# Optimization experiments

Hardware: AMD Instinct MI355X
Metric: run time of the kernel (lower is better)

Reference implementation:

```python
import jax, jax.numpy as jnp
import numpy as np

E = 5        # num_experts
K = 2        # top-k routing
DIM = 768    # token dim
HID = 3072   # dim * mlp_ratio
T = 16384    # num tokens (batch*seq collapsed, per SparseDispatcher contract)
EPS = float(np.finfo(np.float64).eps)  # np.finfo(float).eps used in combine


def setup_inputs() -> dict:
    key = jax.random.key(0)
    ks = jax.random.split(key, 5)
    x = jax.random.normal(ks[0], (T, DIM), jnp.float32)
    # w_gate is nn.Parameter(zeros) in the source; randomize so routing is non-trivial
    w_gate = jax.random.normal(ks[1], (DIM, E), jnp.float32) * 0.02
    # stacked ExpertMLP params (fc1: dim->hid, fc2: hid->dim), small init per init_weights
    W1 = jax.random.normal(ks[2], (E, DIM, HID), jnp.float32) * 0.02
    b1 = jnp.zeros((E, HID), jnp.float32)
    W2 = jax.random.normal(ks[3], (E, HID, DIM), jnp.float32) * 0.02
    b2 = jnp.zeros((E, DIM), jnp.float32)
    return {"x": x, "w_gate": w_gate, "W1": W1, "b1": b1, "W2": W2, "b2": b2}


def reference(x, w_gate, W1, b1, W2, b2):
    # --- noisy top-k gating, eval mode (no noise added at inference) ---
    logits = x @ w_gate                              # [T, E]
    top_vals, top_idx = jax.lax.top_k(logits, K)     # [T, K]
    top_gates = jax.nn.softmax(top_vals, axis=-1)    # softmax over selected logits
    tok = jnp.arange(x.shape[0])[:, None]
    gates = jnp.zeros_like(logits).at[tok, top_idx].set(top_gates)  # sparse [T, E]

    # --- dispatch / expert MLP / combine ---
    # SparseDispatcher.combine: combined[b] = log(sum_e gate[b,e] * exp(expert_e(x[b])))
    # (zeros where no expert contributes are replaced by eps before log)
    acc = jnp.zeros((x.shape[0], DIM), jnp.float32)
    for e in range(E):  # small fixed expert count; dense-equivalent of sparse dispatch
        h = jax.nn.gelu(x @ W1[e] + b1[e], approximate=False)  # torch nn.GELU (erf)
        y = h @ W2[e] + b2[e]                                   # [T, DIM]
        acc = acc + gates[:, e:e + 1] * jnp.exp(y)
    return jnp.log(jnp.where(acc == 0.0, EPS, acc))
```

## Files before the change

### kernel.cpp

```cpp
#include <hip/hip_runtime.h>
#include <math.h>

#define T_TOK 16384
#define DIM   768
#define HID   3072
#define NE    5
#define MT    65
#define HCAP  (MT * 128)
#define CSTR  32
#define EPSF  2.2204460492503131e-16f

typedef short bf16x8  __attribute__((ext_vector_type(8)));
typedef float f32x4   __attribute__((ext_vector_type(4)));
typedef float f32x16  __attribute__((ext_vector_type(16)));

#define MFMA16(A, B, C) __builtin_amdgcn_mfma_f32_16x16x32_bf16((A), (B), (C), 0, 0, 0)
#define MFMA32(A, B, C) __builtin_amdgcn_mfma_f32_32x32x16_bf16((A), (B), (C), 0, 0, 0)

__device__ __forceinline__ unsigned short f2bf(float f) {
    unsigned int u = __float_as_uint(f);
    unsigned int r = (u + 0x7fffu + ((u >> 16) & 1u)) >> 16;
    return (unsigned short)r;
}

__device__ __forceinline__ void gld16(const void* g, void* l) {
    __builtin_amdgcn_global_load_lds(
        (const __attribute__((address_space(1))) void*)g,
        (__attribute__((address_space(3))) void*)l, 16, 0, 0);
}

__global__ void prep_w1p(const float* __restrict__ W1, unsigned short* __restrict__ W1p) {
    int idx = blockIdx.x * 256 + threadIdx.x;
    if (idx >= NE * 24 * 12 * 128 * 8) return;
    int p = idx & 7;
    int n = (idx >> 3) & 127;
    int t = idx >> 10;
    int kb = t % 12; t /= 12;
    int nb = t % 24; int e = t / 24;
    int klog = kb * 64 + (p ^ (n & 7)) * 8;
    const float* src = W1 + ((size_t)e * DIM + klog) * HID + nb * 128 + n;
    bf16x8 v;
    #pragma unroll
    for (int j = 0; j < 8; ++j) v[j] = (short)f2bf(src[(size_t)j * HID]);
    *reinterpret_cast<bf16x8*>(W1p + (size_t)idx * 8) = v;
}

__global__ void prep_w2p(const float* __restrict__ W2, unsigned short* __restrict__ W2p) {
    int idx = blockIdx.x * 256 + threadIdx.x;
    if (idx >= NE * 6 * 48 * 128 * 8) return;
    int p = idx & 7;
    int n = (idx >> 3) & 127;
    int t = idx >> 10;
    int kb = t % 48; t /= 48;
    int nb = t % 6; int e = t / 6;
    int klog = kb * 64 + (p ^ (n & 7)) * 8;
    const float* src = W2 + ((size_t)e * HID + klog) * DIM + nb * 128 + n;
    bf16x8 v;
    #pragma unroll
    for (int j = 0; j < 8; ++j) v[j] = (short)f2bf(src[(size_t)j * DIM]);
    *reinterpret_cast<bf16x8*>(W2p + (size_t)idx * 8) = v;
}

__global__ __launch_bounds__(256) void gate_kernel(
    const float* __restrict__ x, const float* __restrict__ wg,
    unsigned short* __restrict__ xb, int* __restrict__ counts,
    int* __restrict__ btok, float* __restrict__ bgate) {
    __shared__ int   s_e[2][64];
    __shared__ float s_g[2][64];
    __shared__ int   lcnt[NE];
    __shared__ int   gbase[NE];

    const int tid = threadIdx.x;
    if (tid < NE) lcnt[tid] = 0;
    const int grp = tid >> 4, l16 = tid & 15;
    const int t0 = blockIdx.x * 64 + grp * 4;

    double acc[4][NE];
    #pragma unroll
    for (int tt = 0; tt < 4; ++tt)
        #pragma unroll
        for (int e = 0; e < NE; ++e) acc[tt][e] = 0.0;

    for (int i = 0; i < 12; ++i) {
        const int dbase = i * 64 + l16 * 4;
        float4 xv[4];
        #pragma unroll
        for (int tt = 0; tt < 4; ++tt) {
            xv[tt] = *reinterpret_cast<const float4*>(x + (size_t)(t0 + tt) * DIM + dbase);
            ushort4 o;
            o.x = f2bf(xv[tt].x); o.y = f2bf(xv[tt].y);
            o.z = f2bf(xv[tt].z); o.w = f2bf(xv[tt].w);
            *reinterpret_cast<ushort4*>(xb + (size_t)(t0 + tt) * DIM + dbase) = o;
        }
        #pragma unroll
        for (int j = 0; j < 4; ++j) {
            const int d = dbase + j;
            float w0 = wg[d * NE + 0], w1 = wg[d * NE + 1], w2 = wg[d * NE + 2];
            float w3 = wg[d * NE + 3], w4 = wg[d * NE + 4];
            #pragma unroll
            for (int tt = 0; tt < 4; ++tt) {
                double xd = (double)((&xv[tt].x)[j]);
                acc[tt][0] += xd * (double)w0;
                acc[tt][1] += xd * (double)w1;
                acc[tt][2] += xd * (double)w2;
                acc[tt][3] += xd * (double)w3;
                acc[tt][4] += xd * (double)w4;
            }
        }
    }
    #pragma unroll
    for (int off = 8; off; off >>= 1)
        #pragma unroll
        for (int tt = 0; tt < 4; ++tt)
            #pragma unroll
            for (int e = 0; e < NE; ++e)
                acc[tt][e] += __shfl_down(acc[tt][e], off, 16);

    if (l16 == 0) {
        #pragma unroll
        for (int tt = 0; tt < 4; ++tt) {
            double v[NE] = {acc[tt][0], acc[tt][1], acc[tt][2], acc[tt][3], acc[tt][4]};
            int i0 = 0;
            for (int e = 1; e < NE; ++e) if (v[e] > v[i0]) i0 = e;
            int i1 = -1;
            for (int e = 0; e < NE; ++e) {
                if (e == i0) continue;
                if (i1 < 0 || v[e] > v[i1]) i1 = e;
            }
            float e1 = expf((float)(v[i1] - v[i0]));
            float g0 = 1.0f / (1.0f + e1);
            int li = grp * 4 + tt;
            s_e[0][li] = i0;  s_g[0][li] = g0;
            s_e[1][li] = i1;  s_g[1][li] = e1 * g0;
        }
    }
    __syncthreads();

    int mye = 0, myoff = 0, mytok = 0;
    float myg = 0.0f;
    if (tid < 128) {
        int li = tid >> 1, which = tid & 1;
        mye = s_e[which][li];
        myg = s_g[which][li];
        mytok = blockIdx.x * 64 + li;
        myoff = atomicAdd(&lcnt[mye], 1);
    }
    __syncthreads();
    if (tid < NE) gbase[tid] = atomicAdd(&counts[tid * CSTR], lcnt[tid]);
    __syncthreads();
    if (tid < 128) {
        int p = gbase[mye] + myoff;
        btok[mye * T_TOK + p] = mytok;
        bgate[mye * T_TOK + p] = myg;
    }
}

__global__ __launch_bounds__(256, 3) void combo_kernel(
    const unsigned short* __restrict__ xb,
    const unsigned short* __restrict__ W1p,
    const unsigned short* __restrict__ W2p,
    const float* __restrict__ b1, const float* __restrict__ b2,
    const int* __restrict__ counts, const int* __restrict__ btok,
    const float* __restrict__ bgate,
    unsigned short* __restrict__ h0, unsigned short* __restrict__ h1,
    float* __restrict__ out, int g1e, int g2e) {
    __shared__ __align__(16) unsigned short As[128 * 64];
    __shared__ __align__(16) unsigned short Bs[128 * 64];
    __shared__ int   sst[128];
    __shared__ float ssg[128];

    const int g2n = (g2e >= 0) ? MT * 6 : 0;
    int bx = blockIdx.x;
    const bool isG2 = bx < g2n;
    int e, mt, nt;
    if (isG2) { e = g2e; mt = bx / 6;  nt = bx % 6; }
    else      { bx -= g2n; e = g1e; mt = bx / 24; nt = bx % 24; }
    const int cnt = counts[e * CSTR];
    const int m0 = mt * 128;
    if (m0 >= cnt) return;
    unsigned short* hbuf = (e & 1) ? h1 : h0;

    const int tid = threadIdx.x;
    const int wv = tid >> 6, lane = tid & 63;
    const int wm = wv >> 1, wn = wv & 1;
    const int col = lane & 15, quad = lane >> 4;
    const int l8 = lane & 7, r8 = lane >> 3;

    const unsigned short* aptr[4];
    if (isG2) {
        if (tid < 128) {
            int pos = m0 + tid;
            sst[tid] = (pos < cnt) ? btok[e * T_TOK + pos] : 0;
            ssg[tid] = (pos < cnt) ? bgate[e * T_TOK + pos] : 0.0f;
        }
        #pragma unroll
        for (int q = 0; q < 4; ++q) {
            int r = wv * 32 + q * 8 + r8;
            aptr[q] = hbuf + (size_t)(m0 + r) * HID + (l8 ^ r8) * 8;
        }
    } else {
        #pragma unroll
        for (int q = 0; q < 4; ++q) {
            int r = wv * 32 + q * 8 + r8;
            int pos = m0 + r;
            int tok = btok[e * T_TOK + (pos < cnt ? pos : 0)];
            aptr[q] = xb + (size_t)tok * DIM + (l8 ^ r8) * 8;
        }
    }
    const unsigned short* btile = isG2
        ? W2p + ((size_t)(e * 6 + nt)) * 48 * 8192
        : W1p + ((size_t)(e * 24 + nt)) * 12 * 8192;
    const int ksteps = isG2 ? 48 : 12;

    f32x4 acc[4][4];
    #pragma unroll
    for (int i = 0; i < 4; ++i)
        #pragma unroll
        for (int j = 0; j < 4; ++j)
            acc[i][j] = (f32x4){0.f, 0.f, 0.f, 0.f};

    for (int ks = 0; ks < ksteps; ++ks) {
        const unsigned short* bk = btile + (size_t)ks * 8192 + (size_t)wv * 2048 + lane * 8;
        #pragma unroll
        for (int q = 0; q < 4; ++q)
            gld16(aptr[q] + ks * 64, &As[(wv * 4 + q) * 512]);
        #pragma unroll
        for (int q = 0; q < 4; ++q)
            gld16(bk + q * 512, &Bs[(wv * 4 + q) * 512]);
        __syncthreads();
        #pragma unroll
        for (int kf = 0; kf < 2; ++kf) {
            const int p = ((kf * 4 + quad) ^ l8) * 8;
            bf16x8 a[4], b[4];
            #pragma unroll
            for (int i = 0; i < 4; ++i)
                a[i] = *reinterpret_cast<const bf16x8*>(&As[(wm * 64 + i * 16 + col) * 64 + p]);
            #pragma unroll
            for (int i = 0; i < 4; ++i)
                b[i] = *reinterpret_cast<const bf16x8*>(&Bs[(wn * 64 + i * 16 + col) * 64 + p]);
            #pragma unroll
            for (int i = 0; i < 4; ++i)
                #pragma unroll
                for (int j = 0; j < 4; ++j)
                    acc[i][j] = MFMA16(a[i], b[j], acc[i][j]);
        }
        __syncthreads();
    }

    const int nb0 = nt * 128 + wn * 64;
    if (!isG2) {
        #pragma unroll
        for (int j = 0; j < 4; ++j) {
            float bias = b1[e * HID + nb0 + j * 16 + col];
            #pragma unroll
            for (int i = 0; i < 4; ++i) {
                #pragma unroll
                for (int r = 0; r < 4; ++r) {
                    int row = m0 + wm * 64 + i * 16 + quad * 4 + r;
                    float v = acc[i][j][r] + bias;
                    float gl = 0.5f * v * (1.0f + erff(v * 0.70710678118654752f));
                    hbuf[(size_t)row * HID + nb0 + j * 16 + col] = f2bf(gl);
                }
            }
        }
    } else {
        #pragma unroll
        for (int j = 0; j < 4; ++j) {
            float bias = b2[e * DIM + nb0 + j * 16 + col];
            #pragma unroll
            for (int i = 0; i < 4; ++i) {
                #pragma unroll
                for (int r = 0; r < 4; ++r) {
                    int lrow = wm * 64 + i * 16 + quad * 4 + r;
                    float g = ssg[lrow];
                    if (g > 0.0f) {
                        float v = acc[i][j][r] + bias;
                        atomicAdd(out + (size_t)sst[lrow] * DIM + nb0 + j * 16 + col,
                                  g * expf(v));
                    }
                }
            }
        }
    }
}

__global__ void log_kernel(float* __restrict__ out, int n) {
    int i = blockIdx.x * 256 + threadIdx.x;
    if (i < n) {
        float v = out[i];
        out[i] = logf(v == 0.0f ? EPSF : v);
    }
}

__global__ void prep_w1_v2(const float* __restrict__ W1, unsigned short* __restrict__ W1s) {
    int g = blockIdx.x * 4 + (threadIdx.x >> 6);
    int lane = threadIdx.x & 63;
    int kf = g % 48;
    int rest = g / 48;
    int nt2 = rest % 96;
    int e = rest / 96;
    int n = nt2 * 32 + (lane & 31);
    int k0 = kf * 16 + (lane >> 5) * 8;
    const float* src = W1 + ((size_t)e * DIM + k0) * HID + n;
    bf16x8 v;
    #pragma unroll
    for (int j = 0; j < 8; ++j) v[j] = (short)f2bf(src[(size_t)j * HID]);
    *reinterpret_cast<bf16x8*>(W1s + ((size_t)g * 64 + lane) * 8) = v;
}

__global__ void prep_w2_v2(const float* __restrict__ W2, unsigned short* __restrict__ W2s) {
    int g = blockIdx.x * 4 + (threadIdx.x >> 6);
    int lane = threadIdx.x & 63;
    int kf = g % 192;
    int rest = g / 192;
    int nt2 = rest % 24;
    int e = rest / 24;
    int n = nt2 * 32 + (lane & 31);
    int k0 = kf * 16 + (lane >> 5) * 8;
    const float* src = W2 + ((size_t)e * HID + k0) * DIM + n;
    bf16x8 v;
    #pragma unroll
    for (int j = 0; j < 8; ++j) v[j] = (short)f2bf(src[(size_t)j * DIM]);
    *reinterpret_cast<bf16x8*>(W2s + ((size_t)g * 64 + lane) * 8) = v;
}

__global__ __launch_bounds__(512, 2) void expert_v2(
    const unsigned short* __restrict__ xb, const unsigned short* __restrict__ W1s,
    const unsigned short* __restrict__ W2s, const float* __restrict__ b1,
    const float* __restrict__ b2, const int* __restrict__ counts,
    const int* __restrict__ btok, const float* __restrict__ bgate,
    float* __restrict__ out) {
    __shared__ __align__(16) unsigned short xs[64][776];
    __shared__ __align__(16) unsigned short hs[2][64][136];
    __shared__ int   st[64];
    __shared__ float sg[64];

    const int e = blockIdx.y;
    const int cnt = counts[e * CSTR];
    const int m0 = blockIdx.x * 64;
    if (m0 >= cnt) return;

    const int tid = threadIdx.x;
    const int wv = tid >> 6, lane = tid & 63;
    const int l31 = lane & 31, lhi = lane >> 5;

    if (tid < 64) {
        int pos = m0 + tid;
        st[tid] = (pos < cnt) ? btok[e * T_TOK + pos] : 0;
        sg[tid] = (pos < cnt) ? bgate[e * T_TOK + pos] : 0.0f;
    }
    __syncthreads();
    {
        int r = tid >> 3, seg = tid & 7;
        const unsigned short* src = xb + (size_t)st[r] * DIM + seg * 96;
        unsigned short* dst = &xs[r][seg * 96];
        #pragma unroll
        for (int i = 0; i < 12; ++i)
            reinterpret_cast<bf16x8*>(dst)[i] = reinterpret_cast<const bf16x8*>(src)[i];
    }
    __syncthreads();

    const int mt2 = wv & 1, nt2l = wv >> 1;
    f32x16 acc[2][3];
    #pragma unroll
    for (int a_ = 0; a_ < 2; ++a_)
        #pragma unroll
        for (int b_ = 0; b_ < 3; ++b_)
            #pragma unroll
            for (int q = 0; q < 16; ++q) acc[a_][b_][q] = 0.0f;

    const unsigned short* arow = &xs[mt2 * 32 + l31][lhi * 8];
    for (int jc = 0; jc < 24; ++jc) {
        f32x16 c0, c1;
        #pragma unroll
        for (int q = 0; q < 16; ++q) { c0[q] = 0.0f; c1[q] = 0.0f; }
        const unsigned short* bpa =
            W1s + ((size_t)((e * 96 + jc * 4 + nt2l) * 48)) * 512 + lane * 8;
        #pragma unroll
        for (int kf = 0; kf < 48; kf += 2) {
            bf16x8 a0 = *reinterpret_cast<const bf16x8*>(arow + kf * 16);
            bf16x8 b0 = *reinterpret_cast<const bf16x8*>(bpa + (size_t)kf * 512);
            c0 = MFMA32(a0, b0, c0);
            bf16x8 a1 = *reinterpret_cast<const bf16x8*>(arow + kf * 16 + 16);
            bf16x8 b1 = *reinterpret_cast<const bf16x8*>(bpa + (size_t)kf * 512 + 512);
            c1 = MFMA32(a1, b1, c1);
        }
        #pragma unroll
        for (int q = 0; q < 16; ++q) c0[q] += c1[q];
        {
            int colc = nt2l * 32 + l31;
            float bias = b1[e * HID + jc * 128 + colc];
            #pragma unroll
            for (int reg = 0; reg < 16; ++reg) {
                int row = (reg & 3) + 8 * (reg >> 2) + 4 * lhi;
                float v = c0[reg] + bias;
                float gl = 0.5f * v * (1.0f + erff(v * 0.70710678118654752f));
                hs[jc & 1][mt2 * 32 + row][colc] = f2bf(gl);
            }
        }
        __syncthreads();
        const unsigned short* bpb =
            W2s + ((size_t)((e * 24 + wv * 3) * 192 + jc * 8)) * 512 + lane * 8;
        #pragma unroll
        for (int kf = 0; kf < 8; ++kf) {
            bf16x8 af0 = *reinterpret_cast<const bf16x8*>(&hs[jc & 1][l31][kf * 16 + lhi * 8]);
            bf16x8 af1 = *reinterpret_cast<const bf16x8*>(&hs[jc & 1][32 + l31][kf * 16 + lhi * 8]);
            #pragma unroll
            for (int i = 0; i < 3; ++i) {
                bf16x8 bv = *reinterpret_cast<const bf16x8*>(bpb + ((size_t)i * 192 + kf) * 512);
                acc[0][i] = MFMA32(af0, bv, acc[0][i]);
                acc[1][i] = MFMA32(af1, bv, acc[1][i]);
            }
        }
    }
    #pragma unroll
    for (int mt = 0; mt < 2; ++mt) {
        #pragma unroll
        for (int i = 0; i < 3; ++i) {
            int cg = (wv * 3 + i) * 32 + l31;
            float bias2 = b2[e * DIM + cg];
            #pragma unroll
            for (int reg = 0; reg < 16; ++reg) {
                int row = mt * 32 + (reg & 3) + 8 * (reg >> 2) + 4 * lhi;
                float g = sg[row];
                if (g > 0.0f) {
                    float v = acc[mt][i][reg] + bias2;
                    atomicAdd(out + (size_t)st[row] * DIM + cg, g * expf(v));
                }
            }
        }
    }
}


extern "C" void kernel_launch(void* const* d_in, const int* in_sizes, int n_in,
                              void* d_out, int out_size, void* d_ws, size_t ws_size,
                              hipStream_t stream) {
    const float* x  = (const float*)d_in[0];
    const float* wg = (const float*)d_in[1];
    const float* W1 = (const float*)d_in[2];
    const float* b1 = (const float*)d_in[3];
    const float* W2 = (const float*)d_in[4];
    const float* b2 = (const float*)d_in[5];
    float* out = (float*)d_out;

    char* ws = (char*)d_ws;
    int*            counts = (int*)ws;
    int*            btok   = (int*)(ws + 1024);
    float*          bgate  = (float*)(ws + 1024 + 327680);
    unsigned short* xb     = (unsigned short*)(ws + 1024 + 2 * 327680);
    unsigned short* W1b    = xb + (size_t)T_TOK * DIM;
    unsigned short* W2b    = W1b + (size_t)NE * DIM * HID;
    unsigned short* h0     = W2b + (size_t)NE * HID * DIM;
    unsigned short* h1     = h0 + (size_t)HCAP * HID;

    const size_t need_fast = 1024 + 2 * 327680
        + (size_t)T_TOK * DIM * 2 + 2 * (size_t)NE * DIM * HID * 2
        + 2 * (size_t)HCAP * HID * 2;
    const bool fast = ws_size >= need_fast;

    hipMemsetAsync(counts, 0, 1024, stream);
    hipMemsetAsync(out, 0, (size_t)out_size * sizeof(float), stream);

    gate_kernel<<<T_TOK / 64, 256, 0, stream>>>(x, wg, xb, counts, btok, bgate);

    if (fast) {
        prep_w1p<<<(NE * 24 * 12 * 128 * 8 + 255) / 256, 256, 0, stream>>>(W1, W1b);
        prep_w2p<<<(NE * 6 * 48 * 128 * 8 + 255) / 256, 256, 0, stream>>>(W2, W2b);
        for (int s = 0; s < 6; ++s) {
            int g1e = (s <= 4) ? s : -1;
            int g2e = s - 1;
            int nb = (g2e >= 0 ? MT * 6 : 0) + (g1e >= 0 ? MT * 24 : 0);
            combo_kernel<<<nb, 256, 0, stream>>>(xb, W1b, W2b, b1, b2, counts,
                                                 btok, bgate, h0, h1, out, g1e, g2e);
        }
    } else {
        prep_w1_v2<<<NE * 96 * 48 / 4, 256, 0, stream>>>(W1, W1b);
        prep_w2_v2<<<NE * 24 * 192 / 4, 256, 0, stream>>>(W2, W2b);
        expert_v2<<<dim3(T_TOK / 64, NE), 512, 0, stream>>>(
            xb, W1b, W2b, b1, b2, counts, btok, bgate, out);
    }

    log_kernel<<<(out_size + 255) / 256, 256, 0, stream>>>(out, out_size);
}
```

Measured before the change: 716.5 us.

## Triple-buffer LDS pipeline with 256-row tiles and 512-thread blocks in expert GEMM

Raises the expert GEMM tile from 128 to 256 token rows using 8 waves per block. It adds a three-stage LDS ring buffer so global-to-LDS loads for step k+2 overlap the MFMA work on step k, synchronised with explicit vmcnt waits and barriers. It also remaps block indices so that consecutive blocks are spread across tiles, and raises wave priority around the compute phase. The goal is to hide memory latency and improve weight reuse per block. In exchange it uses more LDS per block, allows fewer blocks per CU, and leaves larger tail tiles when experts receive uneven token counts.

New measurement: 885.0 us. 23.5% more time.

```diff
diff --git a/kernel.cpp b/kernel.cpp
--- a/kernel.cpp
+++ b/kernel.cpp
@@ -5,8 +5,10 @@
 #define DIM   768
 #define HID   3072
 #define NE    5
-#define MT    65
-#define HCAP  (MT * 128)
+#define MT2   32
+#define HCAP  (MT2 * 256)
+#define G1NT  24
+#define G2NT  6
 #define CSTR  32
 #define EPSF  2.2204460492503131e-16f
 
@@ -155,7 +157,7 @@
     }
 }
 
-__global__ __launch_bounds__(256, 3) void combo_kernel(
+__global__ __launch_bounds__(512, 2) void combo_kernel(
     const unsigned short* __restrict__ xb,
     const unsigned short* __restrict__ W1p,
     const unsigned short* __restrict__ W2p,
@@ -164,19 +166,27 @@
     const float* __restrict__ bgate,
     unsigned short* __restrict__ h0, unsigned short* __restrict__ h1,
     float* __restrict__ out, int g1e, int g2e) {
-    __shared__ __align__(16) unsigned short As[128 * 64];
-    __shared__ __align__(16) unsigned short Bs[128 * 64];
-    __shared__ int   sst[128];
-    __shared__ float ssg[128];
-
-    const int g2n = (g2e >= 0) ? MT * 6 : 0;
+    __shared__ __align__(16) unsigned short As[3][256 * 64];
+    __shared__ __align__(16) unsigned short Bs[3][128 * 64];
+    __shared__ int   sst[256];
+    __shared__ float ssg[256];
+
+    const int g2n = (g2e >= 0) ? MT2 * G2NT : 0;
     int bx = blockIdx.x;
     const bool isG2 = bx < g2n;
     int e, mt, nt;
-    if (isG2) { e = g2e; mt = bx / 6;  nt = bx % 6; }
-    else      { bx -= g2n; e = g1e; mt = bx / 24; nt = bx % 24; }
+    if (isG2) {
+        e = g2e;
+        int w = (bx & 7) * (g2n >> 3) + (bx >> 3);
+        mt = w / G2NT; nt = w % G2NT;
+    } else {
+        bx -= g2n;
+        e = g1e;
+        int w = (bx & 7) * ((MT2 * G1NT) >> 3) + (bx >> 3);
+        mt = w / G1NT; nt = w % G1NT;
+    }
     const int cnt = counts[e * CSTR];
-    const int m0 = mt * 128;
+    const int m0 = mt * 256;
     if (m0 >= cnt) return;
     unsigned short* hbuf = (e & 1) ? h1 : h0;
 
@@ -188,7 +198,7 @@
 
     const unsigned short* aptr[4];
     if (isG2) {
-        if (tid < 128) {
+        if (tid < 256) {
             int pos = m0 + tid;
             sst[tid] = (pos < cnt) ? btok[e * T_TOK + pos] : 0;
             ssg[tid] = (pos < cnt) ? bgate[e * T_TOK + pos] : 0.0f;
@@ -208,9 +218,19 @@
         }
     }
     const unsigned short* btile = isG2
-        ? W2p + ((size_t)(e * 6 + nt)) * 48 * 8192
-        : W1p + ((size_t)(e * 24 + nt)) * 12 * 8192;
+        ? W2p + ((size_t)(e * G2NT + nt)) * 48 * 8192
+        : W1p + ((size_t)(e * G1NT + nt)) * 12 * 8192;
+    const unsigned short* bsrc = btile + (size_t)wv * 1024 + lane * 8;
     const int ksteps = isG2 ? 48 : 12;
+
+    auto STAGE = [&](int KS, int B_) {
+        #pragma unroll
+        for (int q = 0; q < 4; ++q)
+            gld16(aptr[q] + KS * 64, &As[B_][wv * 2048 + q * 512]);
+        #pragma unroll
+        for (int j = 0; j < 2; ++j)
+            gld16(bsrc + (size_t)KS * 8192 + j * 512, &Bs[B_][wv * 1024 + j * 512]);
+    };
 
     f32x4 acc[4][4];
     #pragma unroll
@@ -219,32 +239,45 @@
         for (int j = 0; j < 4; ++j)
             acc[i][j] = (f32x4){0.f, 0.f, 0.f, 0.f};
 
-    for (int ks = 0; ks < ksteps; ++ks) {
-        const unsigned short* bk = btile + (size_t)ks * 8192 + (size_t)wv * 2048 + lane * 8;
-        #pragma unroll
-        for (int q = 0; q < 4; ++q)
-            gld16(aptr[q] + ks * 64, &As[(wv * 4 + q) * 512]);
-        #pragma unroll
-        for (int q = 0; q < 4; ++q)
-            gld16(bk + q * 512, &Bs[(wv * 4 + q) * 512]);
-        __syncthreads();
+    auto COMPUTE = [&](int B_) {
         #pragma unroll
         for (int kf = 0; kf < 2; ++kf) {
             const int p = ((kf * 4 + quad) ^ l8) * 8;
-            bf16x8 a[4], b[4];
+            bf16x8 a[4], bb[4];
             #pragma unroll
             for (int i = 0; i < 4; ++i)
-                a[i] = *reinterpret_cast<const bf16x8*>(&As[(wm * 64 + i * 16 + col) * 64 + p]);
-            #pragma unroll
-            for (int i = 0; i < 4; ++i)
-                b[i] = *reinterpret_cast<const bf16x8*>(&Bs[(wn * 64 + i * 16 + col) * 64 + p]);
+                a[i] = *reinterpret_cast<const bf16x8*>(&As[B_][(wm * 64 + i * 16 + col) * 64 + p]);
+            #pragma unroll
+            for (int j = 0; j < 4; ++j)
+                bb[j] = *reinterpret_cast<const bf16x8*>(&Bs[B_][(wn * 64 + j * 16 + col) * 64 + p]);
             #pragma unroll
             for (int i = 0; i < 4; ++i)
                 #pragma unroll
                 for (int j = 0; j < 4; ++j)
-                    acc[i][j] = MFMA16(a[i], b[j], acc[i][j]);
-        }
-        __syncthreads();
+                    acc[i][j] = MFMA16(a[i], bb[j], acc[i][j]);
+        }
+    };
+
+    STAGE(0, 0);
+    STAGE(1, 1);
+    asm volatile("s_waitcnt vmcnt(6)" ::: "memory");
+    __builtin_amdgcn_s_barrier();
+    asm volatile("" ::: "memory");
+
+    for (int ks = 0; ks < ksteps; ++ks) {
+        const int b = ks % 3;
+        if (ks + 2 < ksteps) STAGE(ks + 2, (ks + 2) % 3);
+        __builtin_amdgcn_s_setprio(1);
+        COMPUTE(b);
+        __builtin_amdgcn_s_setprio(0);
+        if (ks + 1 < ksteps) {
+            if (ks + 2 < ksteps)
+                asm volatile("s_waitcnt vmcnt(6)" ::: "memory");
+            else
+                asm volatile("s_waitcnt vmcnt(0)" ::: "memory");
+            __builtin_amdgcn_s_barrier();
+            asm volatile("" ::: "memory");
+        }
     }
 
     const int nb0 = nt * 128 + wn * 64;
@@ -470,8 +503,8 @@
         for (int s = 0; s < 6; ++s) {
             int g1e = (s <= 4) ? s : -1;
             int g2e = s - 1;
-            int nb = (g2e >= 0 ? MT * 6 : 0) + (g1e >= 0 ? MT * 24 : 0);
-            combo_kernel<<<nb, 256, 0, stream>>>(xb, W1b, W2b, b1, b2, counts,
+            int nb = (g2e >= 0 ? MT2 * G2NT : 0) + (g1e >= 0 ? MT2 * G1NT : 0);
+            combo_kernel<<<nb, 512, 0, stream>>>(xb, W1b, W2b, b1, b2, counts,
                                                  btok, bgate, h0, h1, out, g1e, g2e);
         }
     } else {
```
